# Performance work log

Hardware: AMD Instinct MI355X
Metric: run time of the kernel (lower is better)

## Reference

```python
import jax, jax.numpy as jnp
import numpy as np
import itertools

G = 24  # octahedral rotation group order (reflection=False)
K = 3   # kernel_size

def _octahedral_tables():
    # 24 proper rotations of the cube as signed permutation matrices (det=+1)
    mats = []
    for perm in itertools.permutations(range(3)):
        for signs in itertoolsools_product if False else itertools.product((1, -1), repeat=3):
            M = np.zeros((3, 3), dtype=np.int64)
            for i, p in enumerate(perm):
                M[i, p] = signs[i]
            if round(np.linalg.det(M)) == 1:
                mats.append(M)
    mats = np.stack(mats)  # (24,3,3)
    key = {tuple(m.flatten()): i for i, m in enumerate(mats)}
    # Cayley-derived index shift: shift[g][h] = index of R_g^{-1} R_h
    shift = np.zeros((G, G), dtype=np.int64)
    for g in range(G):
        Rg_inv = mats[g].T  # orthogonal
        for h in range(G):
            shift[g, h] = key[tuple((Rg_inv @ mats[h]).flatten())]
    # spatial rotation gather indices: rotated K'(x) = K(R^{-1}(x-c)+c)
    c = (K - 1) // 2
    coords = np.stack(np.meshgrid(np.arange(K), np.arange(K), np.arange(K), indexing='ij'), -1).reshape(-1, 3)
    rot_idx = np.zeros((G, K ** 3), dtype=np.int64)
    for g in range(G):
        src = (coords - c) @ mats[g]  # equals R_g^{-1} @ (x-c) row-wise
        src = src + c
        rot_idx[g] = src[:, 0] * K * K + src[:, 1] * K + src[:, 2]
    return shift, rot_idx

SHIFT, ROT_IDX = _octahedral_tables()

def setup_inputs() -> dict:
    key = jax.random.key(0)
    k1, k2, k3, k4, k5 = jax.random.split(key, 5)
    B, I, O, H = 2, 16, 16, 32
    fan_g = I  # kaiming-ish scale for g_weight last dim
    fan_t = K ** 3
    return {
        'x': jax.random.normal(k1, (B, I, G, H, H, H), dtype=jnp.float32),
        'g_weight': jax.random.normal(k2, (G, O, I), dtype=jnp.float32) * (1.0 / np.sqrt(fan_g)),
        't_weight': jax.random.normal(k3, (O, 1, K, K, K), dtype=jnp.float32) * (1.0 / np.sqrt(fan_t)),
        'g_bias': jax.random.normal(k4, (1, O, 1, 1, 1, 1), dtype=jnp.float32) * 0.1,
        't_bias': jax.random.normal(k5, (1,), dtype=jnp.float32) * 0.1,
    }

def reference(x, g_weight, t_weight, g_bias, t_bias):
    O = g_weight.shape[1]
    B, _, _, H, W, D = x.shape
    # filter bank G: permute group axis of g_weight per group element -> (G_z, G_g, O, I)
    gfb = g_weight[SHIFT]
    # filter bank T: rotated depthwise kernels -> (O, G, K^3)
    tfb = t_weight.reshape(O, K ** 3)[:, ROT_IDX]
    w = tfb.reshape(O * G, 1, K, K, K)
    # group-equivariant channel mix + bias
    y = jnp.einsum('bighwd,zgoi->bozhwd', x, gfb) + g_bias
    y = y.reshape(B, O * G, H, W, D)
    # depthwise conv3d with groups = O*G, padding=1, stride=1
    out = jax.lax.conv_general_dilated(
        y, w, window_strides=(1, 1, 1), padding=[(1, 1)] * 3,
        dimension_numbers=('NCDHW', 'OIDHW', 'NCDHW'),
        feature_group_count=O * G) + t_bias[0]
    out = out.reshape(B, O, G, out.shape[2], out.shape[3], out.shape[4])
    return jax.nn.leaky_relu(out, negative_slope=0.01)
```

## Files before the change

kernel.cpp:

```cpp
#include <hip/hip_runtime.h>
#include <hip/hip_bf16.h>
#include <stdint.h>

typedef unsigned short ushortx;
typedef __attribute__((ext_vector_type(8))) short bs8;
typedef __attribute__((ext_vector_type(4))) float f32x4;

struct Tab {
    int shift[24][24];
    int rot[24][27];
};

constexpr Tab make_tab() {
    Tab t{};
    int mats[24][3][3] = {};
    {
        const int perms[6][3] = {{0,1,2},{0,2,1},{1,0,2},{1,2,0},{2,0,1},{2,1,0}};
        const int sgns[8][3]  = {{1,1,1},{1,1,-1},{1,-1,1},{1,-1,-1},
                                 {-1,1,1},{-1,1,-1},{-1,-1,1},{-1,-1,-1}};
        int n = 0;
        for (int pi = 0; pi < 6; ++pi)
            for (int si = 0; si < 8; ++si) {
                int M[3][3] = {};
                for (int i = 0; i < 3; ++i) M[i][perms[pi][i]] = sgns[si][i];
                int det = M[0][0]*(M[1][1]*M[2][2]-M[1][2]*M[2][1])
                        - M[0][1]*(M[1][0]*M[2][2]-M[1][2]*M[2][0])
                        + M[0][2]*(M[1][0]*M[2][1]-M[1][1]*M[2][0]);
                if (det == 1) {
                    for (int i = 0; i < 3; ++i)
                        for (int j = 0; j < 3; ++j) mats[n][i][j] = M[i][j];
                    ++n;
                }
            }
    }
    for (int g = 0; g < 24; ++g)
        for (int h = 0; h < 24; ++h) {
            int P[3][3] = {};
            for (int i = 0; i < 3; ++i)
                for (int j = 0; j < 3; ++j) {
                    int s = 0;
                    for (int e = 0; e < 3; ++e) s += mats[g][e][i] * mats[h][e][j];
                    P[i][j] = s;
                }
            for (int k = 0; k < 24; ++k) {
                bool eq = true;
                for (int i = 0; i < 3; ++i)
                    for (int j = 0; j < 3; ++j)
                        if (mats[k][i][j] != P[i][j]) eq = false;
                if (eq) t.shift[g][h] = k;
            }
        }
    for (int g = 0; g < 24; ++g)
        for (int j = 0; j < 27; ++j) {
            int co[3] = { j/9 - 1, (j/3)%3 - 1, j%3 - 1 };
            int src[3] = {};
            for (int d = 0; d < 3; ++d) {
                int s = 0;
                for (int e = 0; e < 3; ++e) s += co[e] * mats[g][e][d];
                src[d] = s + 1;
            }
            t.rot[g][j] = src[0]*9 + src[1]*3 + src[2];
        }
    return t;
}

__constant__ Tab TAB = make_tab();

#define GG 24
#define OO 16
#define II 16
#define PVOL 32768
#define MCH 384
#define KCH 384
#define KG  48

__device__ __forceinline__ unsigned f2bfu(float f) {
    union { float f; unsigned u; } a; a.f = f;
    unsigned r = a.u + 0x7FFFu + ((a.u >> 16) & 1u);
    return r >> 16;
}
__device__ __forceinline__ float bfu2f(unsigned h) {
    union { unsigned u; float f; } a; a.u = h << 16;
    return a.f;
}

#define GLOAD16(gp, lp) \
    __builtin_amdgcn_global_load_lds((const __attribute__((address_space(1))) void*)(gp), \
                                     (__attribute__((address_space(3))) void*)(lp), 16, 0, 0)

__global__ void build_weights2(const float* __restrict__ gw, const float* __restrict__ tw,
                               ushortx* __restrict__ w2, float* __restrict__ wt) {
    int idx = blockIdx.x * 256 + threadIdx.x;
    if (idx < MCH * KCH) {
        int m = idx / KCH, k = idx % KCH;
        int o = m / GG, z = m % GG;
        int i = k / GG, g = k % GG;
        float w = gw[TAB.shift[z][g] * (OO * II) + o * II + i];
        unsigned h = f2bfu(w);
        unsigned l = f2bfu(w - bfu2f(h));
        size_t base = (size_t)m * 768 + (k >> 5) * 64 + (k & 31);
        w2[base]      = (ushortx)h;
        w2[base + 32] = (ushortx)l;
    } else {
        int r = idx - MCH * KCH;
        if (r < MCH * 27) {
            int c = r / 27, j = r % 27;
            wt[r] = tw[(c / GG) * 27 + TAB.rot[c % GG][j]];
        }
    }
}

__global__ __launch_bounds__(256) void convert_x(const float* __restrict__ X,
                                                 uint4* __restrict__ Xhi,
                                                 uint4* __restrict__ Xlo) {
    const int n0 = blockIdx.x * 256, kg = blockIdx.y, b = blockIdx.z;
    __shared__ float s[8][260];
    const int t = threadIdx.x;
    const float* Xb = X + ((size_t)b * KCH + kg * 8) * PVOL;

    {
        const int r0 = t >> 6, c4 = (t & 63) * 4;
        float4 v0 = *(const float4*)&Xb[(size_t)r0 * PVOL + n0 + c4];
        float4 v1 = *(const float4*)&Xb[(size_t)(r0 + 4) * PVOL + n0 + c4];
        *(float4*)&s[r0][c4] = v0;
        *(float4*)&s[r0 + 4][c4] = v1;
    }
    __syncthreads();

    const int n = t;
    float f0 = s[0][n], f1 = s[1][n], f2 = s[2][n], f3 = s[3][n];
    float f4 = s[4][n], f5 = s[5][n], f6 = s[6][n], f7 = s[7][n];

    unsigned h0 = f2bfu(f0), h1 = f2bfu(f1), h2 = f2bfu(f2), h3 = f2bfu(f3);
    unsigned h4 = f2bfu(f4), h5 = f2bfu(f5), h6 = f2bfu(f6), h7 = f2bfu(f7);
    uint4 H = { h0 | (h1 << 16), h2 | (h3 << 16), h4 | (h5 << 16), h6 | (h7 << 16) };

    unsigned l0 = f2bfu(f0 - bfu2f(h0)), l1 = f2bfu(f1 - bfu2f(h1));
    unsigned l2 = f2bfu(f2 - bfu2f(h2)), l3 = f2bfu(f3 - bfu2f(h3));
    unsigned l4 = f2bfu(f4 - bfu2f(h4)), l5 = f2bfu(f5 - bfu2f(h5));
    unsigned l6 = f2bfu(f6 - bfu2f(h6)), l7 = f2bfu(f7 - bfu2f(h7));
    uint4 L = { l0 | (l1 << 16), l2 | (l3 << 16), l4 | (l5 << 16), l6 | (l7 << 16) };

    const size_t ci = ((size_t)(b * KG + kg)) * PVOL + n0 + n;
    Xhi[ci] = H;
    Xlo[ci] = L;
}

__global__ __launch_bounds__(256) void gemm_mfma(const ushortx* __restrict__ W2,
                                                 const uint4* __restrict__ Xhi,
                                                 const uint4* __restrict__ Xlo,
                                                 const float* __restrict__ gbias,
                                                 float* __restrict__ Y) {
    __shared__ ushortx As[8192];
    __shared__ ushortx Bs[8192];
    const int b = blockIdx.z, m0 = blockIdx.y * 128, n0 = blockIdx.x * 128;
    const int tid = threadIdx.x, lane = tid & 63, wave = tid >> 6;
    const int wr = wave >> 1, wc = wave & 1;
    const int l15 = lane & 15, lq = lane >> 4;

    f32x4 acc[4][4] = {};

    const char* Ab = (const char*)W2 + (size_t)m0 * 1536;
    const uint4* XH = Xhi + (size_t)b * KG * PVOL + n0;
    const uint4* XL = Xlo + (size_t)b * KG * PVOL + n0;

    for (int it = 0; it < 12; ++it) {
        #pragma unroll
        for (int j = 0; j < 4; ++j) {
            int inst = j * 4 + wave;
            int fb = inst * 1024 + (lane << 4);
            int row = fb >> 7;
            int slot = (fb >> 4) & 7;
            int sch = slot ^ (row & 7);
            GLOAD16(Ab + (size_t)row * 1536 + it * 128 + sch * 16, (char*)As + fb);
            const uint4* plane = (sch < 4) ? XH : XL;
            GLOAD16(plane + ((size_t)(it * 4 + (sch & 3))) * PVOL + row, (char*)Bs + fb);
        }
        __syncthreads();

        bs8 ah[4], al[4], bh[4], bl[4];
        #pragma unroll
        for (int f = 0; f < 4; ++f) {
            int rowA = wr * 64 + f * 16 + l15;
            int swzA = (rowA & 7) << 4;
            ah[f] = *(const bs8*)((const char*)As + rowA * 128 + ((lq * 16) ^ swzA));
            al[f] = *(const bs8*)((const char*)As + rowA * 128 + ((64 + lq * 16) ^ swzA));
            int rowB = wc * 64 + f * 16 + l15;
            int swzB = (rowB & 7) << 4;
            bh[f] = *(const bs8*)((const char*)Bs + rowB * 128 + ((lq * 16) ^ swzB));
            bl[f] = *(const bs8*)((const char*)Bs + rowB * 128 + ((64 + lq * 16) ^ swzB));
        }
        #pragma unroll
        for (int fm = 0; fm < 4; ++fm)
            #pragma unroll
            for (int fn = 0; fn < 4; ++fn) {
                acc[fm][fn] = __builtin_amdgcn_mfma_f32_16x16x32_bf16(ah[fm], bh[fn], acc[fm][fn], 0, 0, 0);
                acc[fm][fn] = __builtin_amdgcn_mfma_f32_16x16x32_bf16(ah[fm], bl[fn], acc[fm][fn], 0, 0, 0);
                acc[fm][fn] = __builtin_amdgcn_mfma_f32_16x16x32_bf16(al[fm], bh[fn], acc[fm][fn], 0, 0, 0);
            }
        __syncthreads();
    }

    float* Yp = Y + (size_t)b * MCH * PVOL;
    #pragma unroll
    for (int fm = 0; fm < 4; ++fm)
        #pragma unroll
        for (int j = 0; j < 4; ++j) {
            int m = m0 + wr * 64 + fm * 16 + lq * 4 + j;
            float bias = gbias[m / GG];
            #pragma unroll
            for (int fn = 0; fn < 4; ++fn) {
                int n = n0 + wc * 64 + fn * 16 + l15;
                Yp[(size_t)m * PVOL + n] = acc[fm][fn][j] + bias;
            }
        }
}

__global__ __launch_bounds__(256) void dwconv(const float* __restrict__ Y,
                                              const float* __restrict__ Wt,
                                              const float* __restrict__ tb,
                                              float* __restrict__ O) {
    const int x0 = blockIdx.x * 4;
    const int c  = blockIdx.y;
    const int b  = blockIdx.z;
    const float* __restrict__ Yc = Y + ((size_t)(b * MCH + c)) * PVOL;
    float* __restrict__ Oc = O + ((size_t)(b * MCH + c)) * PVOL;

    __shared__ float s[6][34][40];
    __shared__ float taps[27];
    const int t = threadIdx.x;

    {
        float4 z4 = {0.f, 0.f, 0.f, 0.f};
        float4* sp = (float4*)s;
        for (int i = t; i < 2040; i += 256) sp[i] = z4;
    }
    if (t < 27) taps[t] = Wt[c * 27 + t];
    __syncthreads();

    const int y  = t >> 3;
    const int z0 = (t & 7) * 4;

    {
        float4 r[6];
        #pragma unroll
        for (int lx = 0; lx < 6; ++lx) {
            int x = x0 - 1 + lx;
            bool ok = (x >= 0 && x < 32);
            r[lx] = ok ? *(const float4*)&Yc[(size_t)x * 1024 + y * 32 + z0]
                       : (float4){0.f, 0.f, 0.f, 0.f};
        }
        #pragma unroll
        for (int lx = 0; lx < 6; ++lx)
            *(float4*)&s[lx][1 + y][4 + z0] = r[lx];
    }
    __syncthreads();

    const float t0 = tb[0];
    float w[27];
    #pragma unroll
    for (int j = 0; j < 27; ++j) w[j] = taps[j];

    float Wn[3][3][6];

    #define LOADWIN(slot, plane)                                              \
        {                                                                     \
            _Pragma("unroll")                                                 \
            for (int dy = 0; dy < 3; ++dy) {                                  \
                float4 a = *(const float4*)&s[plane][y + dy][z0];             \
                float4 bq = *(const float4*)&s[plane][y + dy][z0 + 4];        \
                float4 cq = *(const float4*)&s[plane][y + dy][z0 + 8];        \
                Wn[slot][dy][0] = a.w;                                        \
                Wn[slot][dy][1] = bq.x; Wn[slot][dy][2] = bq.y;               \
                Wn[slot][dy][3] = bq.z; Wn[slot][dy][4] = bq.w;               \
                Wn[slot][dy][5] = cq.x;                                       \
            }                                                                 \
        }

    LOADWIN(0, 0)
    LOADWIN(1, 1)

    #pragma unroll
    for (int xi = 0; xi < 4; ++xi) {
        LOADWIN((xi + 2) % 3, (xi + 2))
        const int s0 = xi % 3, s1 = (xi + 1) % 3, s2 = (xi + 2) % 3;
        float4 o;
        #pragma unroll
        for (int zz = 0; zz < 4; ++zz) {
            float a0 = 0.f, a1 = 0.f, a2 = 0.f;
            #pragma unroll
            for (int dy = 0; dy < 3; ++dy)
                #pragma unroll
                for (int dc = 0; dc < 3; ++dc) {
                    a0 += Wn[s0][dy][zz + dc] * w[dy * 3 + dc];
                    a1 += Wn[s1][dy][zz + dc] * w[9 + dy * 3 + dc];
                    a2 += Wn[s2][dy][zz + dc] * w[18 + dy * 3 + dc];
                }
            float v = a0 + a1 + a2 + t0;
            o[zz] = (v > 0.f) ? v : 0.01f * v;
        }
        *(float4*)&Oc[(size_t)(x0 + xi) * 1024 + y * 32 + z0] = o;
    }
    #undef LOADWIN
}

__global__ void build_weights(const float* __restrict__ gw, const float* __restrict__ tw,
                              float* __restrict__ wmix, float* __restrict__ wt) {
    int idx = blockIdx.x * 256 + threadIdx.x;
    if (idx < MCH * KCH) {
        int c = idx / KCH, k = idx % KCH;
        int o = c / GG, z = c % GG;
        int i = k / GG, g = k % GG;
        wmix[idx] = gw[TAB.shift[z][g] * (OO * II) + o * II + i];
    } else {
        int r = idx - MCH * KCH;
        if (r < MCH * 27) {
            int c = r / 27, j = r % 27;
            wt[r] = tw[(c / GG) * 27 + TAB.rot[c % GG][j]];
        }
    }
}

#define BM 128
#define BN 128
#define BK 16

__global__ __launch_bounds__(256) void gemm_mix(const float* __restrict__ A,
                                                const float* __restrict__ X,
                                                const float* __restrict__ gbias,
                                                float* __restrict__ Y) {
    const int b  = blockIdx.z;
    const int m0 = blockIdx.y * BM;
    const int n0 = blockIdx.x * BN;
    const float* __restrict__ Bp = X + (size_t)b * KCH * PVOL;
    float* __restrict__ Yp = Y + (size_t)b * MCH * PVOL;

    __shared__ float Ash[BK][BM];
    __shared__ float Bsh[BK][BN];

    const int tid = threadIdx.x;
    const int tx = tid % 16;
    const int ty = tid / 16;

    float acc[8][8] = {};

    for (int k0 = 0; k0 < KCH; k0 += BK) {
        #pragma unroll
        for (int r = 0; r < 2; ++r) {
            int tt = tid + r * 256;
            int m = tt / 4;
            int kk = (tt % 4) * 4;
            float4 v = *(const float4*)&A[(m0 + m) * KCH + k0 + kk];
            Ash[kk + 0][m] = v.x; Ash[kk + 1][m] = v.y;
            Ash[kk + 2][m] = v.z; Ash[kk + 3][m] = v.w;
        }
        #pragma unroll
        for (int r = 0; r < 2; ++r) {
            int tt = tid + r * 256;
            int kk = tt / 32;
            int n = (tt % 32) * 4;
            *(float4*)&Bsh[kk][n] = *(const float4*)&Bp[(size_t)(k0 + kk) * PVOL + n0 + n];
        }
        __syncthreads();
        #pragma unroll
        for (int kk = 0; kk < BK; ++kk) {
            float af[8], bf[8];
            #pragma unroll
            for (int i = 0; i < 4; ++i) {
                af[i]     = Ash[kk][ty * 4 + i];
                af[4 + i] = Ash[kk][64 + ty * 4 + i];
                bf[i]     = Bsh[kk][tx * 4 + i];
                bf[4 + i] = Bsh[kk][64 + tx * 4 + i];
            }
            #pragma unroll
            for (int i = 0; i < 8; ++i)
                #pragma unroll
                for (int j = 0; j < 8; ++j)
                    acc[i][j] += af[i] * bf[j];
        }
        __syncthreads();
    }

    #pragma unroll
    for (int i = 0; i < 8; ++i) {
        int m = m0 + ((i < 4) ? (ty * 4 + i) : (64 + ty * 4 + (i - 4)));
        float bias = gbias[m / GG];
        float4 v0 = { acc[i][0] + bias, acc[i][1] + bias, acc[i][2] + bias, acc[i][3] + bias };
        float4 v1 = { acc[i][4] + bias, acc[i][5] + bias, acc[i][6] + bias, acc[i][7] + bias };
        *(float4*)&Yp[(size_t)m * PVOL + n0 + tx * 4]      = v0;
        *(float4*)&Yp[(size_t)m * PVOL + n0 + 64 + tx * 4] = v1;
    }
}

extern "C" void kernel_launch(void* const* d_in, const int* in_sizes, int n_in,
                              void* d_out, int out_size, void* d_ws, size_t ws_size,
                              hipStream_t stream) {
    const float* x  = (const float*)d_in[0];
    const float* gw = (const float*)d_in[1];
    const float* tw = (const float*)d_in[2];
    const float* gb = (const float*)d_in[3];
    const float* tb = (const float*)d_in[4];
    float* out = (float*)d_out;
    float* ws  = (float*)d_ws;

    float*   wt   = ws;
    ushortx* w2   = (ushortx*)(ws + 10368);
    float*   wmix = ws + 10368;
    float*   y    = ws + 157824;
    uint4*   xhi  = (uint4*)(ws + 25323648);
    uint4*   xlo  = (uint4*)(ws + 37906560);

    const size_t need = (size_t)50489472 * 4;

    if (ws_size >= need) {
        build_weights2<<<dim3(617), dim3(256), 0, stream>>>(gw, tw, w2, wt);
        convert_x<<<dim3(128, KG, 2), dim3(256), 0, stream>>>(x, xhi, xlo);
        gemm_mfma<<<dim3(256, 3, 2), dim3(256), 0, stream>>>(w2, xhi, xlo, gb, y);
    } else {
        build_weights<<<dim3(617), dim3(256), 0, stream>>>(gw, tw, wmix, wt);
        gemm_mix<<<dim3(PVOL / BN, MCH / BM, 2), dim3(256), 0, stream>>>(wmix, x, gb, y);
    }
    dwconv<<<dim3(8, MCH, 2), dim3(256), 0, stream>>>(y, wt, tb, out);
}
```

Baseline: 304.6 us.

## Double-buffer LDS tiles in MFMA GEMM to overlap global loads with compute

Doubles the LDS buffers for the A and B tiles and prefetches the next K-slice with direct-to-LDS loads while the current slice is consumed by MFMAs. Manual vmcnt waits and raw s_barrier calls replace __syncthreads. The aim is to hide global memory latency behind the matrix math. In exchange LDS use per block doubles to 64KB, which may lower occupancy, and the hand-written waitcnt relies on assumptions about how many loads are in flight.

```diff
diff --git a/kernel.cpp b/kernel.cpp
--- a/kernel.cpp
+++ b/kernel.cpp
@@ -151,8 +151,8 @@
                                                  const uint4* __restrict__ Xlo,
                                                  const float* __restrict__ gbias,
                                                  float* __restrict__ Y) {
-    __shared__ ushortx As[8192];
-    __shared__ ushortx Bs[8192];
+    __shared__ ushortx As[2][8192];
+    __shared__ ushortx Bs[2][8192];
     const int b = blockIdx.z, m0 = blockIdx.y * 128, n0 = blockIdx.x * 128;
     const int tid = threadIdx.x, lane = tid & 63, wave = tid >> 6;
     const int wr = wave >> 1, wc = wave & 1;
@@ -164,31 +164,47 @@
     const uint4* XH = Xhi + (size_t)b * KG * PVOL + n0;
     const uint4* XL = Xlo + (size_t)b * KG * PVOL + n0;
 
+#define STAGE(bb, it)                                                          \
+    {                                                                          \
+        _Pragma("unroll")                                                      \
+        for (int j = 0; j < 4; ++j) {                                          \
+            int inst = j * 4 + wave;                                           \
+            int fb = inst * 1024 + (lane << 4);                                \
+            int row = fb >> 7;                                                 \
+            int sch = ((fb >> 4) & 7) ^ (row & 7);                             \
+            GLOAD16(Ab + (size_t)row * 1536 + (it) * 128 + sch * 16,           \
+                    (char*)&As[bb][0] + fb);                                   \
+            const uint4* plane = (sch < 4) ? XH : XL;                          \
+            GLOAD16(plane + ((size_t)((it) * 4 + (sch & 3))) * PVOL + row,     \
+                    (char*)&Bs[bb][0] + fb);                                   \
+        }                                                                      \
+    }
+
+    STAGE(0, 0);
+
+    int cur = 0;
     for (int it = 0; it < 12; ++it) {
-        #pragma unroll
-        for (int j = 0; j < 4; ++j) {
-            int inst = j * 4 + wave;
-            int fb = inst * 1024 + (lane << 4);
-            int row = fb >> 7;
-            int slot = (fb >> 4) & 7;
-            int sch = slot ^ (row & 7);
-            GLOAD16(Ab + (size_t)row * 1536 + it * 128 + sch * 16, (char*)As + fb);
-            const uint4* plane = (sch < 4) ? XH : XL;
-            GLOAD16(plane + ((size_t)(it * 4 + (sch & 3))) * PVOL + row, (char*)Bs + fb);
-        }
-        __syncthreads();
+        if (it < 11) {
+            STAGE(cur ^ 1, it + 1);
+            asm volatile("s_waitcnt vmcnt(8)" ::: "memory");
+        } else {
+            asm volatile("s_waitcnt vmcnt(0)" ::: "memory");
+        }
+        __builtin_amdgcn_sched_barrier(0);
+        __builtin_amdgcn_s_barrier();
+        __builtin_amdgcn_sched_barrier(0);
 
         bs8 ah[4], al[4], bh[4], bl[4];
         #pragma unroll
         for (int f = 0; f < 4; ++f) {
             int rowA = wr * 64 + f * 16 + l15;
             int swzA = (rowA & 7) << 4;
-            ah[f] = *(const bs8*)((const char*)As + rowA * 128 + ((lq * 16) ^ swzA));
-            al[f] = *(const bs8*)((const char*)As + rowA * 128 + ((64 + lq * 16) ^ swzA));
+            ah[f] = *(const bs8*)((const char*)&As[cur][0] + rowA * 128 + ((lq * 16) ^ swzA));
+            al[f] = *(const bs8*)((const char*)&As[cur][0] + rowA * 128 + ((64 + lq * 16) ^ swzA));
             int rowB = wc * 64 + f * 16 + l15;
             int swzB = (rowB & 7) << 4;
-            bh[f] = *(const bs8*)((const char*)Bs + rowB * 128 + ((lq * 16) ^ swzB));
-            bl[f] = *(const bs8*)((const char*)Bs + rowB * 128 + ((64 + lq * 16) ^ swzB));
+            bh[f] = *(const bs8*)((const char*)&Bs[cur][0] + rowB * 128 + ((lq * 16) ^ swzB));
+            bl[f] = *(const bs8*)((const char*)&Bs[cur][0] + rowB * 128 + ((64 + lq * 16) ^ swzB));
         }
         #pragma unroll
         for (int fm = 0; fm < 4; ++fm)
@@ -198,8 +214,13 @@
                 acc[fm][fn] = __builtin_amdgcn_mfma_f32_16x16x32_bf16(ah[fm], bl[fn], acc[fm][fn], 0, 0, 0);
                 acc[fm][fn] = __builtin_amdgcn_mfma_f32_16x16x32_bf16(al[fm], bh[fn], acc[fm][fn], 0, 0, 0);
             }
-        __syncthreads();
-    }
+
+        asm volatile("" ::: "memory");
+        __builtin_amdgcn_s_barrier();
+        asm volatile("" ::: "memory");
+        cur ^= 1;
+    }
+#undef STAGE
 
     float* Yp = Y + (size_t)b * MCH * PVOL;
     #pragma unroll
```

Result: no change. 305.2 us (+0.2%).
